# Kernel tuning notes

Hardware: AMD Instinct MI355X
Metric: run time of the kernel (lower is better)

Reference implementation:

```python
import jax, jax.numpy as jnp
import numpy as np

NUM_HEADS = 16
NUM_KV_HEADS = 4
HEAD_SIZE = 128
SCALE = 1.0 / np.sqrt(128.0).astype(np.float32)
NEG_INF = -1e30


def setup_inputs() -> dict:
    key = jax.random.key(0)
    kq, kk, kv = jax.random.split(key, 3)
    B, S = 2, 2048
    query = jax.random.normal(kq, (B, NUM_HEADS, S, HEAD_SIZE), dtype=jnp.float32)
    k = jax.random.normal(kk, (B, NUM_KV_HEADS, S, HEAD_SIZE), dtype=jnp.float32)
    v = jax.random.normal(kv, (B, NUM_KV_HEADS, S, HEAD_SIZE), dtype=jnp.float32)
    return {"query": query, "key": k, "value": v}


def _attn(query, key, value):
    # query: [B, H, S, D]; key/value: [B, Hkv, S, D]; GQA with group = H // Hkv
    B, H, S, D = query.shape
    Hkv = key.shape[1]
    G = H // Hkv
    q = query.reshape(B, Hkv, G, S, D)
    # scores: [B, Hkv, G, Sq, Sk]
    scores = jnp.einsum('bkgsd,bktd->bkgst', q, key) * jnp.float32(SCALE)
    causal = jnp.tril(jnp.ones((S, S), dtype=bool))  # [Sq, Sk]
    scores = jnp.where(causal, scores, jnp.float32(NEG_INF))
    probs = jax.nn.softmax(scores, axis=-1)
    out = jnp.einsum('bkgst,bktd->bkgsd', probs, value)  # [B, Hkv, G, S, D]
    out = out.reshape(B, H, S, D)
    # transpose(1,2).reshape -> [B, S, H*D]
    return out.transpose(0, 2, 1, 3).reshape(B, S, H * D)


def reference(query, key, value):
    return _attn(query, key, value)
```

## Files before the change

kernel.cpp:

```cpp
#include <hip/hip_runtime.h>


#define S_LEN 2048
#define DH    128
#define NH    16
#define NKVH  4
#define NB    2
#define TQ    128
#define TK    64
#define NQT   (S_LEN / TQ)
#define PROW  72
#define QSCALE 0.12752749610559243f

typedef __attribute__((ext_vector_type(8))) short short8;
typedef __attribute__((ext_vector_type(4))) float f32x4;

#if __has_builtin(__builtin_amdgcn_exp2f)
#define EX2(x) __builtin_amdgcn_exp2f(x)
#else
#define EX2(x) exp2f(x)
#endif

__device__ __forceinline__ unsigned short bf1(float a) {
    union { float f; unsigned u; } x; x.f = a;
    return (unsigned short)((x.u + 0x8000u) >> 16);
}
__device__ __forceinline__ unsigned pk2(float a, float b) {
    union { float f; unsigned u; } x, y; x.f = a; y.f = b;
    return ((x.u + 0x8000u) >> 16) | ((y.u + 0x8000u) & 0xffff0000u);
}
__device__ __forceinline__ void cp16(const void* g, void* lds) {
    __builtin_amdgcn_global_load_lds(
        (const __attribute__((address_space(1))) void*)g,
        (__attribute__((address_space(3))) void*)lds, 16, 0, 0);
}

__global__ __launch_bounds__(256, 4)
void prepack(const float* __restrict__ K, const float* __restrict__ V,
             unsigned short* __restrict__ Kb, unsigned short* __restrict__ Vt) {
    if (blockIdx.y == 0) {
        const long long flat = (long long)blockIdx.x * 2048 + threadIdx.x * 8;
        const int s = (int)(flat >> 7) & (S_LEN - 1);
        const int d0 = (int)flat & 127;
        const float* p = K + flat;
        float4 x = *(const float4*)p;
        float4 y = *(const float4*)(p + 4);
        const int cs = (d0 >> 3) ^ (s & 7);
        uint4 o;
        o.x = pk2(x.x, x.y); o.y = pk2(x.z, x.w);
        o.z = pk2(y.x, y.y); o.w = pk2(y.z, y.w);
        *(uint4*)(Kb + (flat & ~127LL) + cs * 8) = o;
    } else {
        const int x = blockIdx.x;
        const int bkvh = x >> 7, sblk = (x >> 2) & 31, q = x & 3;
        const int tid = threadIdx.x;
        __shared__ unsigned Lt[64][17];
        const float* base = V + (size_t)bkvh * S_LEN * DH + (size_t)sblk * 64 * DH + q * 32;
#pragma unroll
        for (int j = 0; j < 2; ++j) {
            const int e = tid + j * 256;
            const int s = e >> 3, c4 = e & 7;
            float4 v = *(const float4*)(base + (size_t)s * DH + c4 * 4);
            Lt[s][c4 * 2]     = pk2(v.x, v.y);
            Lt[s][c4 * 2 + 1] = pk2(v.z, v.w);
        }
        __syncthreads();
        const unsigned short* lt = (const unsigned short*)&Lt[0][0];
        const int d_loc = tid >> 3, pc = tid & 7;
        const int d = q * 32 + d_loc;
        const int c_log = pc ^ (d & 7);
        unsigned short vv[8];
#pragma unroll
        for (int j = 0; j < 8; ++j) {
            const int kp = c_log * 8 + j;
            const int kv = (kp & 3) * 16 + (kp >> 2);
            vv[j] = lt[kv * 34 + d_loc];
        }
        uint4 o;
        o.x = (unsigned)vv[0] | ((unsigned)vv[1] << 16);
        o.y = (unsigned)vv[2] | ((unsigned)vv[3] << 16);
        o.z = (unsigned)vv[4] | ((unsigned)vv[5] << 16);
        o.w = (unsigned)vv[6] | ((unsigned)vv[7] << 16);
        *(uint4*)(Vt + (size_t)bkvh * S_LEN * DH + (size_t)d * S_LEN + sblk * 64 + pc * 8) = o;
    }
}

__global__ __launch_bounds__(256, 2)
void attn_fwd(const float* __restrict__ Q,
              const unsigned short* __restrict__ Kb,
              const unsigned short* __restrict__ Vtg,
              float* __restrict__ O) {
    const int n  = blockIdx.x;
    const int x  = n & 15;
    const int h  = (n >> 4) & 15;
    const int b  = n >> 8;
    const int qt = b ? x : (NQT - 1 - x);
    const int kvh = h >> 2;

    const int tid  = threadIdx.x;
    const int w    = tid >> 6;
    const int lane = tid & 63;
    const int quad = lane >> 4;
    const int l16  = lane & 15;
    const int swz  = l16 & 7;

    __shared__ alignas(16) unsigned short Kl[TK][DH];
    __shared__ alignas(16) unsigned short Vl[DH][TK];
    __shared__ alignas(16) unsigned short Pl[TQ][PROW];

    const unsigned short* kb = Kb  + ((size_t)b * NKVH + kvh) * (size_t)(S_LEN * DH);
    const unsigned short* vb = Vtg + ((size_t)b * NKVH + kvh) * (size_t)(S_LEN * DH);

    const int wq0 = qt * TQ + w * 32;
    short8 aq[2][4];
#pragma unroll
    for (int sub = 0; sub < 2; ++sub) {
        const float* qp = Q + (((size_t)b * NH + h) * S_LEN + wq0 + sub * 16 + l16) * DH;
#pragma unroll
        for (int dc = 0; dc < 4; ++dc) {
            float4 xx = *(const float4*)(qp + dc * 32 + quad * 8);
            float4 yy = *(const float4*)(qp + dc * 32 + quad * 8 + 4);
            union { unsigned u[4]; short8 s; } t;
            t.u[0] = pk2(xx.x * QSCALE, xx.y * QSCALE);
            t.u[1] = pk2(xx.z * QSCALE, xx.w * QSCALE);
            t.u[2] = pk2(yy.x * QSCALE, yy.y * QSCALE);
            t.u[3] = pk2(yy.z * QSCALE, yy.w * QSCALE);
            aq[sub][dc] = t.s;
        }
    }

    f32x4 o[2][8];
#pragma unroll
    for (int sub = 0; sub < 2; ++sub)
#pragma unroll
        for (int ch = 0; ch < 8; ++ch) o[sub][ch] = (f32x4){0.f, 0.f, 0.f, 0.f};
    float lsum[2][4];
#pragma unroll
    for (int sub = 0; sub < 2; ++sub)
#pragma unroll
        for (int r = 0; r < 4; ++r) lsum[sub][r] = 0.f;

    const int nt  = 2 * qt + 2;
    const int ntw = 2 * qt + 1 + (w >> 1);

    for (int t = 0; t < nt; ++t) {
        const int j0 = t * TK;
        __syncthreads();
        {
            const char* ks = (const char*)(kb + (size_t)j0 * DH);
#pragma unroll
            for (int i = 0; i < 4; ++i)
                cp16(ks + w * 4096 + i * 1024 + lane * 16,
                     (char*)&Kl[0][0] + w * 4096 + i * 1024);
            const char* vs = (const char*)vb;
#pragma unroll
            for (int i = 0; i < 4; ++i) {
                const int row  = w * 32 + i * 8 + (lane >> 3);
                const int colB = (lane & 7) * 16;
                cp16(vs + (size_t)row * (S_LEN * 2) + j0 * 2 + colB,
                     (char*)&Vl[0][0] + w * 4096 + i * 1024);
            }
        }
        __syncthreads();

        if (t < ntw) {
            const bool diag = (t == ntw - 1);
            f32x4 s[2][4];
#pragma unroll
            for (int sub = 0; sub < 2; ++sub)
#pragma unroll
                for (int k4 = 0; k4 < 4; ++k4) s[sub][k4] = (f32x4){0.f, 0.f, 0.f, 0.f};
#pragma unroll
            for (int dc = 0; dc < 4; ++dc) {
#pragma unroll
                for (int k4 = 0; k4 < 4; ++k4) {
                    short8 bk = *(const short8*)&Kl[k4 * 16 + l16][((dc * 4 + quad) ^ swz) * 8];
                    s[0][k4] = __builtin_amdgcn_mfma_f32_16x16x32_bf16(aq[0][dc], bk, s[0][k4], 0, 0, 0);
                    s[1][k4] = __builtin_amdgcn_mfma_f32_16x16x32_bf16(aq[1][dc], bk, s[1][k4], 0, 0, 0);
                }
            }
#pragma unroll
            for (int sub = 0; sub < 2; ++sub) {
                const int rb = wq0 + sub * 16 + quad * 4;
#pragma unroll
                for (int r = 0; r < 4; ++r) {
                    float v0 = s[sub][0][r], v1 = s[sub][1][r];
                    float v2 = s[sub][2][r], v3 = s[sub][3][r];
                    if (diag) {
                        const int row = rb + r;
                        if (j0 + l16      > row) v0 = -1e30f;
                        if (j0 + 16 + l16 > row) v1 = -1e30f;
                        if (j0 + 32 + l16 > row) v2 = -1e30f;
                        if (j0 + 48 + l16 > row) v3 = -1e30f;
                    }
                    float p0 = EX2(v0), p1 = EX2(v1), p2 = EX2(v2), p3 = EX2(v3);
                    lsum[sub][r] += (p0 + p1) + (p2 + p3);
                    const int prow = w * 32 + sub * 16 + quad * 4 + r;
                    *(uint2*)&Pl[prow][l16 * 4] = make_uint2(pk2(p0, p1), pk2(p2, p3));
                }
            }
#pragma unroll
            for (int kc = 0; kc < 2; ++kc) {
                short8 ap0 = *(const short8*)&Pl[w * 32 + l16][kc * 32 + quad * 8];
                short8 ap1 = *(const short8*)&Pl[w * 32 + 16 + l16][kc * 32 + quad * 8];
#pragma unroll
                for (int ch = 0; ch < 8; ++ch) {
                    short8 bv = *(const short8*)&Vl[ch * 16 + l16][((kc * 4 + quad) ^ swz) * 8];
                    o[0][ch] = __builtin_amdgcn_mfma_f32_16x16x32_bf16(ap0, bv, o[0][ch], 0, 0, 0);
                    o[1][ch] = __builtin_amdgcn_mfma_f32_16x16x32_bf16(ap1, bv, o[1][ch], 0, 0, 0);
                }
            }
        }
    }

#pragma unroll
    for (int sub = 0; sub < 2; ++sub) {
#pragma unroll
        for (int r = 0; r < 4; ++r) {
            float rs = lsum[sub][r];
            rs += __shfl_xor(rs, 1);
            rs += __shfl_xor(rs, 2);
            rs += __shfl_xor(rs, 4);
            rs += __shfl_xor(rs, 8);
            const float invl = 1.f / rs;
            const int row = wq0 + sub * 16 + quad * 4 + r;
            float* op = O + ((size_t)b * S_LEN + row) * (NH * DH) + h * DH;
#pragma unroll
            for (int ch = 0; ch < 8; ++ch)
                op[ch * 16 + l16] = o[sub][ch][r] * invl;
        }
    }
}

extern "C" void kernel_launch(void* const* d_in, const int* in_sizes, int n_in,
                              void* d_out, int out_size, void* d_ws, size_t ws_size,
                              hipStream_t stream) {
    const float* Q = (const float*)d_in[0];
    const float* K = (const float*)d_in[1];
    const float* V = (const float*)d_in[2];
    float* O = (float*)d_out;
    unsigned short* Kb = (unsigned short*)d_ws;
    unsigned short* Vt = Kb + (size_t)NB * NKVH * S_LEN * DH;
    dim3 pgrid(NB * NKVH * (S_LEN / 16), 2);
    prepack<<<pgrid, 256, 0, stream>>>(K, V, Kb, Vt);
    attn_fwd<<<dim3(512), 256, 0, stream>>>(Q, Kb, Vt, O);
}
```

Before: 153.0 us.

## Double-buffer K tiles and overlap V load with QK compute, swizzle P in LDS

K tiles move into a two-slot LDS buffer, and the next tile is prefetched asynchronously while the current QK^T and softmax run. The V load for the current tile is issued at the top of the iteration and waited on at a single barrier placed before PV. The aim is to hide global-to-LDS latency behind compute. The P buffer loses its padding and uses an XOR swizzle instead, saving LDS and avoiding bank conflicts, at the cost of more LDS use for K and correctness that depends on the async copies completing at the barrier.

```diff
diff --git a/kernel.cpp b/kernel.cpp
--- a/kernel.cpp
+++ b/kernel.cpp
@@ -9,7 +9,6 @@
 #define TQ    128
 #define TK    64
 #define NQT   (S_LEN / TQ)
-#define PROW  72
 #define QSCALE 0.12752749610559243f
 
 typedef __attribute__((ext_vector_type(8))) short short8;
@@ -104,9 +103,9 @@
     const int l16  = lane & 15;
     const int swz  = l16 & 7;
 
-    __shared__ alignas(16) unsigned short Kl[TK][DH];
+    __shared__ alignas(16) unsigned short Kl[2][TK][DH];
     __shared__ alignas(16) unsigned short Vl[DH][TK];
-    __shared__ alignas(16) unsigned short Pl[TQ][PROW];
+    __shared__ alignas(16) unsigned short Pl[TQ][TK];
 
     const unsigned short* kb = Kb  + ((size_t)b * NKVH + kvh) * (size_t)(S_LEN * DH);
     const unsigned short* vb = Vtg + ((size_t)b * NKVH + kvh) * (size_t)(S_LEN * DH);
@@ -143,29 +142,35 @@
     const int nt  = 2 * qt + 2;
     const int ntw = 2 * qt + 1 + (w >> 1);
 
+#pragma unroll
+    for (int i = 0; i < 4; ++i)
+        cp16((const char*)kb + w * 4096 + i * 1024 + lane * 16,
+             (char*)&Kl[0][0][0] + w * 4096 + i * 1024);
+    __syncthreads();
+
     for (int t = 0; t < nt; ++t) {
         const int j0 = t * TK;
-        __syncthreads();
-        {
-            const char* ks = (const char*)(kb + (size_t)j0 * DH);
+#pragma unroll
+        for (int i = 0; i < 4; ++i) {
+            const int row  = w * 32 + i * 8 + (lane >> 3);
+            const int colB = (lane & 7) * 16;
+            cp16((const char*)vb + (size_t)row * (S_LEN * 2) + j0 * 2 + colB,
+                 (char*)&Vl[0][0] + w * 4096 + i * 1024);
+        }
+        if (t + 1 < nt) {
+            const char* ks = (const char*)(kb + (size_t)(j0 + TK) * DH);
+            char* kd = (char*)&Kl[(t + 1) & 1][0][0];
 #pragma unroll
             for (int i = 0; i < 4; ++i)
-                cp16(ks + w * 4096 + i * 1024 + lane * 16,
-                     (char*)&Kl[0][0] + w * 4096 + i * 1024);
-            const char* vs = (const char*)vb;
-#pragma unroll
-            for (int i = 0; i < 4; ++i) {
-                const int row  = w * 32 + i * 8 + (lane >> 3);
-                const int colB = (lane & 7) * 16;
-                cp16(vs + (size_t)row * (S_LEN * 2) + j0 * 2 + colB,
-                     (char*)&Vl[0][0] + w * 4096 + i * 1024);
-            }
-        }
-        __syncthreads();
-
-        if (t < ntw) {
-            const bool diag = (t == ntw - 1);
-            f32x4 s[2][4];
+                cp16(ks + w * 4096 + i * 1024 + lane * 16, kd + w * 4096 + i * 1024);
+        }
+
+        const unsigned short (*Kc)[DH] = Kl[t & 1];
+        const bool active = (t < ntw);
+        const bool diag = (t == ntw - 1);
+        f32x4 s[2][4];
+
+        if (active) {
 #pragma unroll
             for (int sub = 0; sub < 2; ++sub)
 #pragma unroll
@@ -174,7 +179,7 @@
             for (int dc = 0; dc < 4; ++dc) {
 #pragma unroll
                 for (int k4 = 0; k4 < 4; ++k4) {
-                    short8 bk = *(const short8*)&Kl[k4 * 16 + l16][((dc * 4 + quad) ^ swz) * 8];
+                    short8 bk = *(const short8*)&Kc[k4 * 16 + l16][((dc * 4 + quad) ^ swz) * 8];
                     s[0][k4] = __builtin_amdgcn_mfma_f32_16x16x32_bf16(aq[0][dc], bk, s[0][k4], 0, 0, 0);
                     s[1][k4] = __builtin_amdgcn_mfma_f32_16x16x32_bf16(aq[1][dc], bk, s[1][k4], 0, 0, 0);
                 }
@@ -196,13 +201,21 @@
                     float p0 = EX2(v0), p1 = EX2(v1), p2 = EX2(v2), p3 = EX2(v3);
                     lsum[sub][r] += (p0 + p1) + (p2 + p3);
                     const int prow = w * 32 + sub * 16 + quad * 4 + r;
-                    *(uint2*)&Pl[prow][l16 * 4] = make_uint2(pk2(p0, p1), pk2(p2, p3));
+                    const int chs = (l16 >> 1) ^ (prow & 7);
+                    *(uint2*)&Pl[prow][chs * 8 + (l16 & 1) * 4] =
+                        make_uint2(pk2(p0, p1), pk2(p2, p3));
                 }
             }
+        }
+
+        __syncthreads();
+
+        if (active) {
 #pragma unroll
             for (int kc = 0; kc < 2; ++kc) {
-                short8 ap0 = *(const short8*)&Pl[w * 32 + l16][kc * 32 + quad * 8];
-                short8 ap1 = *(const short8*)&Pl[w * 32 + 16 + l16][kc * 32 + quad * 8];
+                const int pr0 = w * 32 + l16;
+                short8 ap0 = *(const short8*)&Pl[pr0][(((kc * 4 + quad) ^ swz)) * 8];
+                short8 ap1 = *(const short8*)&Pl[pr0 + 16][(((kc * 4 + quad) ^ swz)) * 8];
 #pragma unroll
                 for (int ch = 0; ch < 8; ++ch) {
                     short8 bv = *(const short8*)&Vl[ch * 16 + l16][((kc * 4 + quad) ^ swz) * 8];
@@ -211,6 +224,8 @@
                 }
             }
         }
+
+        __syncthreads();
     }
 
 #pragma unroll
```

Result: slower. 158.6 us (+3.7%).
